# Optimization experiments

Hardware: AMD Instinct MI355X
Metric: run time of the kernel (lower is better)

## Reference

```python
import jax, jax.numpy as jnp
import numpy as np

NEG_SLOPE = 0.2
N_NODES = 50000


def _gat_layer(x, src, dst, invalid, W, al, ar, b):
    # x: [N, Fin]; src/dst: [E] (self-loops appended); invalid: [E] bool
    N = x.shape[0]
    H, F = al.shape
    z = (x @ W).reshape(N, H, F)                       # [N,H,F]
    el = jnp.sum(z * al[None], axis=-1)                # [N,H]
    er = jnp.sum(z * ar[None], axis=-1)                # [N,H]
    e = el[src] + er[dst]                              # [E,H]
    e = jnp.where(e > 0, e, NEG_SLOPE * e)             # LeakyReLU(0.2)
    e = jnp.where(invalid[:, None], -jnp.inf, e)       # removed self-loop edges
    # edge softmax per destination node (every node has a self-loop -> max finite)
    m = jax.ops.segment_max(e, dst, num_segments=N)    # [N,H]
    ex = jnp.exp(e - m[dst])
    ex = jnp.where(invalid[:, None], 0.0, ex)
    s = jax.ops.segment_sum(ex, dst, num_segments=N)   # [N,H]
    alpha = ex / s[dst]                                # [E,H]
    msg = z[src] * alpha[:, :, None]                   # [E,H,F]
    out = jax.ops.segment_sum(msg, dst, num_segments=N)  # [N,H,F]
    out = out + b.reshape(1, H, F)
    return jax.nn.elu(out)


def _with_self_loops(src, dst):
    N = N_NODES
    loop = jnp.arange(N, dtype=src.dtype)
    invalid = jnp.concatenate([src == dst, jnp.zeros(N, dtype=bool)])
    return jnp.concatenate([src, loop]), jnp.concatenate([dst, loop]), invalid


def setup_inputs() -> dict:
    key = jax.random.key(0)
    ks = jax.random.split(key, 12)
    N, Fin, H0, F0, H1, C = N_NODES, 256, 4, 32, 1, 40
    E = 800000
    sc = lambda k, shp, fan: jax.random.normal(k, shp, jnp.float32) * (1.0 / np.sqrt(fan))
    return {
        "x": jax.random.normal(ks[0], (N, Fin), jnp.float32),
        "src": jax.random.randint(ks[1], (E,), 0, N, jnp.int32),
        "dst": jax.random.randint(ks[2], (E,), 0, N, jnp.int32),
        "W0": sc(ks[3], (Fin, H0 * F0), Fin),
        "al0": sc(ks[4], (H0, F0), F0),
        "ar0": sc(ks[5], (H0, F0), F0),
        "b0": jnp.zeros((H0 * F0,), jnp.float32),
        "W1": sc(ks[6], (H0 * F0, H1 * C), H0 * F0),
        "al1": sc(ks[7], (H1, C), C),
        "ar1": sc(ks[8], (H1, C), C),
        "b1": jnp.zeros((C,), jnp.float32),
    }


def reference(x, src, dst, W0, al0, ar0, b0, W1, al1, ar1, b1):
    s, d, invalid = _with_self_loops(src, dst)
    h = _gat_layer(x, s, d, invalid, W0, al0, ar0, b0)   # [N,4,32]
    h = h.reshape(h.shape[0], -1)                        # flatten(1) -> [N,128]
    h = _gat_layer(h, s, d, invalid, W1, al1, ar1, b1)   # [N,1,40]
    return h.mean(axis=1)                                # mean over heads -> [N,40]
```

## Files before the change

### kernel.cpp

```cpp
#include <hip/hip_runtime.h>
#include <stdint.h>

#define NN 50000
#define EE 800000
#define CAP 96
#define NXCD 8
#define NPX 6250
#define EPB 2048
#define NCHUNK 391

typedef __bf16 bf16x8 __attribute__((ext_vector_type(8)));
typedef float  f32x4  __attribute__((ext_vector_type(4)));

__device__ __forceinline__ float bflo(unsigned int w){ union{unsigned int i;float f;}c; c.i=w<<16; return c.f; }
__device__ __forceinline__ float bfhi(unsigned int w){ union{unsigned int i;float f;}c; c.i=w&0xFFFF0000u; return c.f; }
__device__ __forceinline__ bf16x8 bf8_zero(){
  bf16x8 v;
  #pragma unroll
  for (int j=0;j<8;++j) v[j]=(__bf16)0.f;
  return v;
}

__global__ void k_init(int* __restrict__ cursor, int* __restrict__ csrv){
  int i = blockIdx.x*256 + threadIdx.x;
  if (i < NN){
    cursor[i] = 1;
    csrv[(size_t)i*CAP] = i;
  }
}

__global__ __launch_bounds__(256) void k_scatter(const int* __restrict__ src,
    const int* __restrict__ dst, int* __restrict__ cursor, int* __restrict__ csrv){
  const int xcd = blockIdx.x & 7;
  const int chunk = blockIdx.x >> 3;
  const int lo = xcd*NPX, hi = lo + NPX;
  int e = chunk*EPB + threadIdx.x;
  #pragma unroll
  for (int it=0; it<EPB/256; ++it, e += 256){
    if (e < EE){
      int d = dst[e];
      if (d >= lo && d < hi){
        int s = src[e];
        unsigned int inv = (s==d) ? 0x80000000u : 0u;
        int pos = atomicAdd(&cursor[d], 1);
        csrv[(size_t)d*CAP + pos] = (int)((unsigned int)s | inv);
      }
    }
  }
}

__global__ __launch_bounds__(256) void k_prepW0(const float* __restrict__ W0,
                                                __bf16* __restrict__ Wg){
  int tg = blockIdx.x*256 + threadIdx.x;
  if (tg >= 4096) return;
  int k8 = tg >> 7, n = tg & 127;
  bf16x8 v;
  #pragma unroll
  for (int j=0;j<8;++j) v[j] = (__bf16)W0[(k8*8+j)*128 + n];
  *(bf16x8*)(Wg + ((size_t)(k8*128 + n))*8) = v;
}

__global__ __launch_bounds__(256) void k_gemm0(const float* __restrict__ x,
    const __bf16* __restrict__ Wg, const float* __restrict__ al0, const float* __restrict__ ar0,
    __bf16* __restrict__ z0b, float* __restrict__ el0, float* __restrict__ er0){
  const int tid = threadIdx.x;
  const int wv = tid >> 6, ln = tid & 63, q = ln >> 4, mr = ln & 15;
  const int nhalf = wv & 1, mhalf = wv >> 1;
  const int m0w = blockIdx.x*64 + mhalf*32;
  const int n0w = nhalf*64;
  f32x4 acc[2][4];
  #pragma unroll
  for (int mt=0;mt<2;++mt)
    #pragma unroll
    for (int nt=0;nt<4;++nt) acc[mt][nt] = (f32x4){0.f,0.f,0.f,0.f};
  const bool av0 = (m0w + mr) < NN;
  const bool av1 = (m0w + 16 + mr) < NN;
  const float* xr0 = x + (size_t)(m0w + mr)*256;
  const float* xr1 = x + (size_t)(m0w + 16 + mr)*256;
  #pragma unroll
  for (int kc=0;kc<8;++kc){
    int ko = kc*32 + q*8;
    bf16x8 a0 = bf8_zero(), a1 = bf8_zero();
    if (av0){
      float4 p = *(const float4*)(xr0 + ko);
      float4 p2 = *(const float4*)(xr0 + ko + 4);
      a0[0]=(__bf16)p.x; a0[1]=(__bf16)p.y; a0[2]=(__bf16)p.z; a0[3]=(__bf16)p.w;
      a0[4]=(__bf16)p2.x; a0[5]=(__bf16)p2.y; a0[6]=(__bf16)p2.z; a0[7]=(__bf16)p2.w;
    }
    if (av1){
      float4 p = *(const float4*)(xr1 + ko);
      float4 p2 = *(const float4*)(xr1 + ko + 4);
      a1[0]=(__bf16)p.x; a1[1]=(__bf16)p.y; a1[2]=(__bf16)p.z; a1[3]=(__bf16)p.w;
      a1[4]=(__bf16)p2.x; a1[5]=(__bf16)p2.y; a1[6]=(__bf16)p2.z; a1[7]=(__bf16)p2.w;
    }
    const __bf16* wb = Wg + ((size_t)((kc*4+q)*128 + n0w + mr))*8;
    #pragma unroll
    for (int nt=0;nt<4;++nt){
      bf16x8 bf = *(const bf16x8*)(wb + (size_t)nt*16*8);
      acc[0][nt] = __builtin_amdgcn_mfma_f32_16x16x32_bf16(a0, bf, acc[0][nt], 0,0,0);
      acc[1][nt] = __builtin_amdgcn_mfma_f32_16x16x32_bf16(a1, bf, acc[1][nt], 0,0,0);
    }
  }
  float alv[4], arv[4];
  #pragma unroll
  for (int nt=0;nt<4;++nt){ int c = n0w + nt*16 + mr; alv[nt]=al0[c]; arv[nt]=ar0[c]; }
  #pragma unroll
  for (int mt=0;mt<2;++mt){
    #pragma unroll
    for (int r=0;r<4;++r){
      int grow = m0w + mt*16 + q*4 + r;
      if (grow < NN){
        #pragma unroll
        for (int nt=0;nt<4;++nt)
          z0b[(size_t)grow*128 + n0w + nt*16 + mr] = (__bf16)acc[mt][nt][r];
      }
      float pl0 = acc[mt][0][r]*alv[0] + acc[mt][1][r]*alv[1];
      float pr0 = acc[mt][0][r]*arv[0] + acc[mt][1][r]*arv[1];
      float pl1 = acc[mt][2][r]*alv[2] + acc[mt][3][r]*alv[3];
      float pr1 = acc[mt][2][r]*arv[2] + acc[mt][3][r]*arv[3];
      #pragma unroll
      for (int off=1; off<16; off<<=1){
        pl0 += __shfl_xor(pl0, off, 16); pr0 += __shfl_xor(pr0, off, 16);
        pl1 += __shfl_xor(pl1, off, 16); pr1 += __shfl_xor(pr1, off, 16);
      }
      if (mr==0 && grow<NN){
        el0[grow*4 + 2*nhalf]   = pl0; er0[grow*4 + 2*nhalf]   = pr0;
        el0[grow*4 + 2*nhalf+1] = pl1; er0[grow*4 + 2*nhalf+1] = pr1;
      }
    }
  }
}

__global__ __launch_bounds__(256) void k_agg0(const unsigned short* __restrict__ z0b,
    const float* __restrict__ el0, const float* __restrict__ er0,
    const int* __restrict__ cursor, const int* __restrict__ csrv,
    const float* __restrict__ b0, unsigned short* __restrict__ hb){
  int lane = threadIdx.x & 63;
  int i = blockIdx.x*4 + (threadIdx.x >> 6);
  int h1 = lane >> 4;
  float erv = er0[i*4 + h1];
  float ax=0.f, ay=0.f, s=0.f;
  int p = i*CAP, pe = p + cursor[i];
  for (; p+4<=pe; p+=4){
    int v0=csrv[p], v1=csrv[p+1], v2=csrv[p+2], v3=csrv[p+3];
    int u0=v0&0x7FFFFFFF, u1=v1&0x7FFFFFFF, u2=v2&0x7FFFFFFF, u3=v3&0x7FFFFFFF;
    float l0=el0[u0*4+h1], l1=el0[u1*4+h1], l2=el0[u2*4+h1], l3=el0[u3*4+h1];
    unsigned int zw0 = *(const unsigned int*)(z0b + (size_t)u0*128 + (lane<<1));
    unsigned int zw1 = *(const unsigned int*)(z0b + (size_t)u1*128 + (lane<<1));
    unsigned int zw2 = *(const unsigned int*)(z0b + (size_t)u2*128 + (lane<<1));
    unsigned int zw3 = *(const unsigned int*)(z0b + (size_t)u3*128 + (lane<<1));
    float e0=l0+erv; e0 = e0>0.f?e0:0.2f*e0; float w0 = v0>=0 ? __expf(e0) : 0.f;
    float e1=l1+erv; e1 = e1>0.f?e1:0.2f*e1; float w1 = v1>=0 ? __expf(e1) : 0.f;
    float e2=l2+erv; e2 = e2>0.f?e2:0.2f*e2; float w2 = v2>=0 ? __expf(e2) : 0.f;
    float e3=l3+erv; e3 = e3>0.f?e3:0.2f*e3; float w3 = v3>=0 ? __expf(e3) : 0.f;
    s += (w0+w1)+(w2+w3);
    ax = fmaf(w0, bflo(zw0), ax); ay = fmaf(w0, bfhi(zw0), ay);
    ax = fmaf(w1, bflo(zw1), ax); ay = fmaf(w1, bfhi(zw1), ay);
    ax = fmaf(w2, bflo(zw2), ax); ay = fmaf(w2, bfhi(zw2), ay);
    ax = fmaf(w3, bflo(zw3), ax); ay = fmaf(w3, bfhi(zw3), ay);
  }
  for (; p<pe; ++p){
    int v=csrv[p]; int u=v&0x7FFFFFFF;
    float l=el0[u*4+h1];
    unsigned int zw = *(const unsigned int*)(z0b + (size_t)u*128 + (lane<<1));
    float e=l+erv; e = e>0.f?e:0.2f*e; float w = v>=0 ? __expf(e) : 0.f;
    s += w; ax = fmaf(w, bflo(zw), ax); ay = fmaf(w, bfhi(zw), ay);
  }
  float inv = 1.f/s;
  float ox = ax*inv + b0[lane*2], oy = ay*inv + b0[lane*2+1];
  ox = ox>0.f?ox:__expf(ox)-1.f; oy = oy>0.f?oy:__expf(oy)-1.f;
  union { __bf16 b[2]; unsigned int u; } pk;
  pk.b[0]=(__bf16)ox; pk.b[1]=(__bf16)oy;
  *(unsigned int*)(hb + (size_t)i*128 + (lane<<1)) = pk.u;
}

__global__ __launch_bounds__(256) void k_gemm1(const __bf16* __restrict__ hb,
    const float* __restrict__ W1, const float* __restrict__ al1, const float* __restrict__ ar1,
    __bf16* __restrict__ z1b, float* __restrict__ el1, float* __restrict__ er1){
  __shared__ __bf16 Blds[16][48][8];
  const int tid = threadIdx.x;
  for (int t=tid; t<16*48*8; t+=256) (&Blds[0][0][0])[t] = (__bf16)0.f;
  __syncthreads();
  for (int t=tid; t<5120; t+=256){
    int k = t/40, n = t - k*40;
    Blds[k>>3][n][k&7] = (__bf16)W1[t];
  }
  __syncthreads();
  const int wm = tid >> 6, ln = tid & 63, q = ln >> 4, mr = ln & 15;
  const int m0 = blockIdx.x*64 + wm*16;
  const int arow = m0 + mr;
  const bool av = (arow < NN);
  f32x4 acc[3];
  #pragma unroll
  for (int nt=0;nt<3;++nt) acc[nt] = (f32x4){0.f,0.f,0.f,0.f};
  #pragma unroll
  for (int kc=0;kc<4;++kc){
    bf16x8 af = bf8_zero();
    if (av) af = *(const bf16x8*)(hb + (size_t)arow*128 + kc*32 + q*8);
    #pragma unroll
    for (int nt=0;nt<3;++nt){
      bf16x8 bf = *(const bf16x8*)&Blds[kc*4+q][nt*16+mr][0];
      acc[nt] = __builtin_amdgcn_mfma_f32_16x16x32_bf16(af, bf, acc[nt], 0,0,0);
    }
  }
  float alv[3], arv[3];
  #pragma unroll
  for (int nt=0;nt<3;++nt){
    int c = nt*16+mr;
    alv[nt] = (c<40) ? al1[c] : 0.f;
    arv[nt] = (c<40) ? ar1[c] : 0.f;
  }
  #pragma unroll
  for (int r=0;r<4;++r){
    int grow = m0 + q*4 + r;
    if (grow < NN){
      #pragma unroll
      for (int nt=0;nt<3;++nt){
        int c = nt*16+mr;
        if (c < 40) z1b[(size_t)grow*40 + c] = (__bf16)acc[nt][r];
      }
    }
    float pl = acc[0][r]*alv[0] + acc[1][r]*alv[1] + acc[2][r]*alv[2];
    float pr = acc[0][r]*arv[0] + acc[1][r]*arv[1] + acc[2][r]*arv[2];
    #pragma unroll
    for (int off=1; off<16; off<<=1){ pl += __shfl_xor(pl, off, 16); pr += __shfl_xor(pr, off, 16); }
    if (mr==0 && grow<NN){ el1[grow]=pl; er1[grow]=pr; }
  }
}

__global__ __launch_bounds__(256) void k_agg1(const unsigned short* __restrict__ z1b,
    const float* __restrict__ el1, const float* __restrict__ er1,
    const int* __restrict__ cursor, const int* __restrict__ csrv,
    const float* __restrict__ b1, float* __restrict__ out){
  int lane = threadIdx.x & 63;
  int i = blockIdx.x*4 + (threadIdx.x >> 6);
  int fl = (lane < 20) ? lane : 0;
  float eri = er1[i];
  float ax=0.f, ay=0.f, s=0.f;
  int p = i*CAP, pe = p + cursor[i];
  for (; p+4<=pe; p+=4){
    int v0=csrv[p], v1=csrv[p+1], v2=csrv[p+2], v3=csrv[p+3];
    int u0=v0&0x7FFFFFFF, u1=v1&0x7FFFFFFF, u2=v2&0x7FFFFFFF, u3=v3&0x7FFFFFFF;
    float l0=el1[u0], l1=el1[u1], l2=el1[u2], l3=el1[u3];
    unsigned int zw0 = *(const unsigned int*)(z1b + (size_t)u0*40 + (fl<<1));
    unsigned int zw1 = *(const unsigned int*)(z1b + (size_t)u1*40 + (fl<<1));
    unsigned int zw2 = *(const unsigned int*)(z1b + (size_t)u2*40 + (fl<<1));
    unsigned int zw3 = *(const unsigned int*)(z1b + (size_t)u3*40 + (fl<<1));
    float e0=l0+eri; e0=e0>0.f?e0:0.2f*e0; float w0 = v0>=0 ? __expf(e0) : 0.f;
    float e1=l1+eri; e1=e1>0.f?e1:0.2f*e1; float w1 = v1>=0 ? __expf(e1) : 0.f;
    float e2=l2+eri; e2=e2>0.f?e2:0.2f*e2; float w2 = v2>=0 ? __expf(e2) : 0.f;
    float e3=l3+eri; e3=e3>0.f?e3:0.2f*e3; float w3 = v3>=0 ? __expf(e3) : 0.f;
    s += (w0+w1)+(w2+w3);
    ax = fmaf(w0, bflo(zw0), ax); ay = fmaf(w0, bfhi(zw0), ay);
    ax = fmaf(w1, bflo(zw1), ax); ay = fmaf(w1, bfhi(zw1), ay);
    ax = fmaf(w2, bflo(zw2), ax); ay = fmaf(w2, bfhi(zw2), ay);
    ax = fmaf(w3, bflo(zw3), ax); ay = fmaf(w3, bfhi(zw3), ay);
  }
  for (; p<pe; ++p){
    int v=csrv[p]; int u=v&0x7FFFFFFF;
    float l=el1[u];
    unsigned int zw = *(const unsigned int*)(z1b + (size_t)u*40 + (fl<<1));
    float e=l+eri; e=e>0.f?e:0.2f*e; float w = v>=0 ? __expf(e) : 0.f;
    s += w; ax = fmaf(w, bflo(zw), ax); ay = fmaf(w, bfhi(zw), ay);
  }
  if (lane < 20){
    float inv = 1.f/s;
    float ox = ax*inv + b1[lane*2], oy = ay*inv + b1[lane*2+1];
    ox = ox>0.f?ox:__expf(ox)-1.f; oy = oy>0.f?oy:__expf(oy)-1.f;
    *(float2*)(out + (size_t)i*40 + (lane<<1)) = make_float2(ox, oy);
  }
}

extern "C" void kernel_launch(void* const* d_in, const int* in_sizes, int n_in,
                              void* d_out, int out_size, void* d_ws, size_t ws_size,
                              hipStream_t stream){
  const float* x   = (const float*)d_in[0];
  const int*   src = (const int*)d_in[1];
  const int*   dst = (const int*)d_in[2];
  const float* W0  = (const float*)d_in[3];
  const float* al0 = (const float*)d_in[4];
  const float* ar0 = (const float*)d_in[5];
  const float* b0  = (const float*)d_in[6];
  const float* W1  = (const float*)d_in[7];
  const float* al1 = (const float*)d_in[8];
  const float* ar1 = (const float*)d_in[9];
  const float* b1  = (const float*)d_in[10];
  float* out = (float*)d_out;

  __bf16* z0b = (__bf16*)d_ws;
  __bf16* hb  = z0b + (size_t)NN*128;
  __bf16* z1b = hb  + (size_t)NN*128;
  __bf16* Wg  = z1b + (size_t)NN*40;
  float* el0 = (float*)(Wg + 32768);
  float* er0 = el0 + (size_t)NN*4;
  float* el1 = er0 + (size_t)NN*4;
  float* er1 = el1 + NN;
  int* cursor = (int*)(er1 + NN);
  int* csrv   = cursor + NN;

  k_prepW0 <<<16, 256, 0, stream>>>(W0, Wg);
  k_init   <<<(NN+255)/256, 256, 0, stream>>>(cursor, csrv);
  k_scatter<<<NCHUNK*NXCD, 256, 0, stream>>>(src, dst, cursor, csrv);

  k_gemm0<<<(NN+63)/64, 256, 0, stream>>>(x, Wg, al0, ar0, z0b, el0, er0);
  k_agg0 <<<NN/4, 256, 0, stream>>>((const unsigned short*)z0b, el0, er0, cursor, csrv, b0, (unsigned short*)hb);
  k_gemm1<<<(NN+63)/64, 256, 0, stream>>>(hb, W1, al1, ar1, z1b, el1, er1);
  k_agg1 <<<NN/4, 256, 0, stream>>>((const unsigned short*)z1b, el1, er1, cursor, csrv, b1, out);
}
```

Measured before the change: 263.4 us.

## Precompute layer-0 edge attention weights during scatter and shrink per-node capacity

The CSR bucket init moves into the first GEMM, and the edge scatter now runs after that GEMM. The scatter then computes the four per-head exp(LeakyReLU) edge weights and stores them as bf16 next to each CSR slot, so the layer-0 aggregation no longer gathers el0 by source or evaluates exp per lane. Aggregation loops unroll by 8, and the per-node capacity drops from 96 to 48 to shrink the CSR footprint. The risks are bf16 rounding of the unnormalised weights, buffer overflow if any node's in-degree plus its self-loop exceeds 48, and a serial dependency that stops the scatter from overlapping the GEMM.

```diff
diff --git a/kernel.cpp b/kernel.cpp
--- a/kernel.cpp
+++ b/kernel.cpp
@@ -3,7 +3,7 @@
 
 #define NN 50000
 #define EE 800000
-#define CAP 96
+#define CAP 48
 #define NXCD 8
 #define NPX 6250
 #define EPB 2048
@@ -14,39 +14,12 @@
 
 __device__ __forceinline__ float bflo(unsigned int w){ union{unsigned int i;float f;}c; c.i=w<<16; return c.f; }
 __device__ __forceinline__ float bfhi(unsigned int w){ union{unsigned int i;float f;}c; c.i=w&0xFFFF0000u; return c.f; }
+__device__ __forceinline__ float bfs(unsigned short u){ union{unsigned int i;float f;}c; c.i=((unsigned int)u)<<16; return c.f; }
 __device__ __forceinline__ bf16x8 bf8_zero(){
   bf16x8 v;
   #pragma unroll
   for (int j=0;j<8;++j) v[j]=(__bf16)0.f;
   return v;
-}
-
-__global__ void k_init(int* __restrict__ cursor, int* __restrict__ csrv){
-  int i = blockIdx.x*256 + threadIdx.x;
-  if (i < NN){
-    cursor[i] = 1;
-    csrv[(size_t)i*CAP] = i;
-  }
-}
-
-__global__ __launch_bounds__(256) void k_scatter(const int* __restrict__ src,
-    const int* __restrict__ dst, int* __restrict__ cursor, int* __restrict__ csrv){
-  const int xcd = blockIdx.x & 7;
-  const int chunk = blockIdx.x >> 3;
-  const int lo = xcd*NPX, hi = lo + NPX;
-  int e = chunk*EPB + threadIdx.x;
-  #pragma unroll
-  for (int it=0; it<EPB/256; ++it, e += 256){
-    if (e < EE){
-      int d = dst[e];
-      if (d >= lo && d < hi){
-        int s = src[e];
-        unsigned int inv = (s==d) ? 0x80000000u : 0u;
-        int pos = atomicAdd(&cursor[d], 1);
-        csrv[(size_t)d*CAP + pos] = (int)((unsigned int)s | inv);
-      }
-    }
-  }
 }
 
 __global__ __launch_bounds__(256) void k_prepW0(const float* __restrict__ W0,
@@ -62,7 +35,8 @@
 
 __global__ __launch_bounds__(256) void k_gemm0(const float* __restrict__ x,
     const __bf16* __restrict__ Wg, const float* __restrict__ al0, const float* __restrict__ ar0,
-    __bf16* __restrict__ z0b, float* __restrict__ el0, float* __restrict__ er0){
+    __bf16* __restrict__ z0b, float* __restrict__ el0, float* __restrict__ er0,
+    unsigned short* __restrict__ wt, int* __restrict__ cursor, int* __restrict__ csrv){
   const int tid = threadIdx.x;
   const int wv = tid >> 6, ln = tid & 63, q = ln >> 4, mr = ln & 15;
   const int nhalf = wv & 1, mhalf = wv >> 1;
@@ -117,7 +91,7 @@
       float pl0 = acc[mt][0][r]*alv[0] + acc[mt][1][r]*alv[1];
       float pr0 = acc[mt][0][r]*arv[0] + acc[mt][1][r]*arv[1];
       float pl1 = acc[mt][2][r]*alv[2] + acc[mt][3][r]*alv[3];
-      float pr1 = acc[mt][2][r]*arv[2] + acc[mt][3][r]*arv[3];
+      float pr1 = acc[mt][3][r]*arv[3] + acc[mt][2][r]*arv[2];
       #pragma unroll
       for (int off=1; off<16; off<<=1){
         pl0 += __shfl_xor(pl0, off, 16); pr0 += __shfl_xor(pr0, off, 16);
@@ -126,44 +100,82 @@
       if (mr==0 && grow<NN){
         el0[grow*4 + 2*nhalf]   = pl0; er0[grow*4 + 2*nhalf]   = pr0;
         el0[grow*4 + 2*nhalf+1] = pl1; er0[grow*4 + 2*nhalf+1] = pr1;
+        float e0 = pl0 + pr0; e0 = e0>0.f ? e0 : 0.2f*e0;
+        float e1 = pl1 + pr1; e1 = e1>0.f ? e1 : 0.2f*e1;
+        union { __bf16 b[2]; unsigned int u; } pk;
+        pk.b[0]=(__bf16)__expf(e0); pk.b[1]=(__bf16)__expf(e1);
+        *(unsigned int*)(wt + ((size_t)grow*CAP)*4 + 2*nhalf) = pk.u;
+        if (nhalf==0){ csrv[(size_t)grow*CAP] = grow; cursor[grow] = 1; }
+      }
+    }
+  }
+}
+
+__global__ __launch_bounds__(256) void k_scatter(const int* __restrict__ src,
+    const int* __restrict__ dst, const float* __restrict__ el0, const float* __restrict__ er0,
+    int* __restrict__ cursor, int* __restrict__ csrv, unsigned short* __restrict__ wt){
+  const int xcd = blockIdx.x & 7;
+  const int chunk = blockIdx.x >> 3;
+  const int lo = xcd*NPX, hi = lo + NPX;
+  int e = chunk*EPB + threadIdx.x;
+  #pragma unroll
+  for (int it=0; it<EPB/256; ++it, e += 256){
+    if (e < EE){
+      int d = dst[e];
+      if (d >= lo && d < hi){
+        int s = src[e];
+        bool inv = (s==d);
+        float4 ls = *(const float4*)(el0 + (size_t)s*4);
+        float4 rd = *(const float4*)(er0 + (size_t)d*4);
+        float e0=ls.x+rd.x; e0 = e0>0.f?e0:0.2f*e0;
+        float e1=ls.y+rd.y; e1 = e1>0.f?e1:0.2f*e1;
+        float e2=ls.z+rd.z; e2 = e2>0.f?e2:0.2f*e2;
+        float e3=ls.w+rd.w; e3 = e3>0.f?e3:0.2f*e3;
+        float w0 = inv?0.f:__expf(e0), w1 = inv?0.f:__expf(e1);
+        float w2 = inv?0.f:__expf(e2), w3 = inv?0.f:__expf(e3);
+        int pos = atomicAdd(&cursor[d], 1);
+        size_t slot = (size_t)d*CAP + pos;
+        csrv[slot] = (int)((unsigned int)s | (inv?0x80000000u:0u));
+        union { __bf16 b[4]; uint2 u; } pk;
+        pk.b[0]=(__bf16)w0; pk.b[1]=(__bf16)w1; pk.b[2]=(__bf16)w2; pk.b[3]=(__bf16)w3;
+        *(uint2*)(wt + slot*4) = pk.u;
       }
     }
   }
 }
 
 __global__ __launch_bounds__(256) void k_agg0(const unsigned short* __restrict__ z0b,
-    const float* __restrict__ el0, const float* __restrict__ er0,
+    const unsigned short* __restrict__ wt,
     const int* __restrict__ cursor, const int* __restrict__ csrv,
     const float* __restrict__ b0, unsigned short* __restrict__ hb){
   int lane = threadIdx.x & 63;
   int i = blockIdx.x*4 + (threadIdx.x >> 6);
   int h1 = lane >> 4;
-  float erv = er0[i*4 + h1];
+  int lane2 = lane << 1;
   float ax=0.f, ay=0.f, s=0.f;
   int p = i*CAP, pe = p + cursor[i];
+  for (; p+8<=pe; p+=8){
+    #pragma unroll
+    for (int j=0;j<8;++j){
+      int u = csrv[p+j] & 0x7FFFFFFF;
+      float w = bfs(wt[(size_t)(p+j)*4 + h1]);
+      unsigned int zw = *(const unsigned int*)(z0b + (size_t)u*128 + lane2);
+      s += w; ax = fmaf(w, bflo(zw), ax); ay = fmaf(w, bfhi(zw), ay);
+    }
+  }
   for (; p+4<=pe; p+=4){
-    int v0=csrv[p], v1=csrv[p+1], v2=csrv[p+2], v3=csrv[p+3];
-    int u0=v0&0x7FFFFFFF, u1=v1&0x7FFFFFFF, u2=v2&0x7FFFFFFF, u3=v3&0x7FFFFFFF;
-    float l0=el0[u0*4+h1], l1=el0[u1*4+h1], l2=el0[u2*4+h1], l3=el0[u3*4+h1];
-    unsigned int zw0 = *(const unsigned int*)(z0b + (size_t)u0*128 + (lane<<1));
-    unsigned int zw1 = *(const unsigned int*)(z0b + (size_t)u1*128 + (lane<<1));
-    unsigned int zw2 = *(const unsigned int*)(z0b + (size_t)u2*128 + (lane<<1));
-    unsigned int zw3 = *(const unsigned int*)(z0b + (size_t)u3*128 + (lane<<1));
-    float e0=l0+erv; e0 = e0>0.f?e0:0.2f*e0; float w0 = v0>=0 ? __expf(e0) : 0.f;
-    float e1=l1+erv; e1 = e1>0.f?e1:0.2f*e1; float w1 = v1>=0 ? __expf(e1) : 0.f;
-    float e2=l2+erv; e2 = e2>0.f?e2:0.2f*e2; float w2 = v2>=0 ? __expf(e2) : 0.f;
-    float e3=l3+erv; e3 = e3>0.f?e3:0.2f*e3; float w3 = v3>=0 ? __expf(e3) : 0.f;
-    s += (w0+w1)+(w2+w3);
-    ax = fmaf(w0, bflo(zw0), ax); ay = fmaf(w0, bfhi(zw0), ay);
-    ax = fmaf(w1, bflo(zw1), ax); ay = fmaf(w1, bfhi(zw1), ay);
-    ax = fmaf(w2, bflo(zw2), ax); ay = fmaf(w2, bfhi(zw2), ay);
-    ax = fmaf(w3, bflo(zw3), ax); ay = fmaf(w3, bfhi(zw3), ay);
+    #pragma unroll
+    for (int j=0;j<4;++j){
+      int u = csrv[p+j] & 0x7FFFFFFF;
+      float w = bfs(wt[(size_t)(p+j)*4 + h1]);
+      unsigned int zw = *(const unsigned int*)(z0b + (size_t)u*128 + lane2);
+      s += w; ax = fmaf(w, bflo(zw), ax); ay = fmaf(w, bfhi(zw), ay);
+    }
   }
   for (; p<pe; ++p){
-    int v=csrv[p]; int u=v&0x7FFFFFFF;
-    float l=el0[u*4+h1];
-    unsigned int zw = *(const unsigned int*)(z0b + (size_t)u*128 + (lane<<1));
-    float e=l+erv; e = e>0.f?e:0.2f*e; float w = v>=0 ? __expf(e) : 0.f;
+    int u = csrv[p] & 0x7FFFFFFF;
+    float w = bfs(wt[(size_t)p*4 + h1]);
+    unsigned int zw = *(const unsigned int*)(z0b + (size_t)u*128 + lane2);
     s += w; ax = fmaf(w, bflo(zw), ax); ay = fmaf(w, bfhi(zw), ay);
   }
   float inv = 1.f/s;
@@ -171,7 +183,7 @@
   ox = ox>0.f?ox:__expf(ox)-1.f; oy = oy>0.f?oy:__expf(oy)-1.f;
   union { __bf16 b[2]; unsigned int u; } pk;
   pk.b[0]=(__bf16)ox; pk.b[1]=(__bf16)oy;
-  *(unsigned int*)(hb + (size_t)i*128 + (lane<<1)) = pk.u;
+  *(unsigned int*)(hb + (size_t)i*128 + lane2) = pk.u;
 }
 
 __global__ __launch_bounds__(256) void k_gemm1(const __bf16* __restrict__ hb,
@@ -234,32 +246,34 @@
     const float* __restrict__ b1, float* __restrict__ out){
   int lane = threadIdx.x & 63;
   int i = blockIdx.x*4 + (threadIdx.x >> 6);
-  int fl = (lane < 20) ? lane : 0;
+  int fl = (lane < 20) ? (lane<<1) : 0;
   float eri = er1[i];
   float ax=0.f, ay=0.f, s=0.f;
   int p = i*CAP, pe = p + cursor[i];
+  for (; p+8<=pe; p+=8){
+    #pragma unroll
+    for (int j=0;j<8;++j){
+      int v=csrv[p+j]; int u=v&0x7FFFFFFF;
+      float l=el1[u];
+      unsigned int zw = *(const unsigned int*)(z1b + (size_t)u*40 + fl);
+      float e=l+eri; e=e>0.f?e:0.2f*e; float w = v>=0 ? __expf(e) : 0.f;
+      s += w; ax = fmaf(w, bflo(zw), ax); ay = fmaf(w, bfhi(zw), ay);
+    }
+  }
   for (; p+4<=pe; p+=4){
-    int v0=csrv[p], v1=csrv[p+1], v2=csrv[p+2], v3=csrv[p+3];
-    int u0=v0&0x7FFFFFFF, u1=v1&0x7FFFFFFF, u2=v2&0x7FFFFFFF, u3=v3&0x7FFFFFFF;
-    float l0=el1[u0], l1=el1[u1], l2=el1[u2], l3=el1[u3];
-    unsigned int zw0 = *(const unsigned int*)(z1b + (size_t)u0*40 + (fl<<1));
-    unsigned int zw1 = *(const unsigned int*)(z1b + (size_t)u1*40 + (fl<<1));
-    unsigned int zw2 = *(const unsigned int*)(z1b + (size_t)u2*40 + (fl<<1));
-    unsigned int zw3 = *(const unsigned int*)(z1b + (size_t)u3*40 + (fl<<1));
-    float e0=l0+eri; e0=e0>0.f?e0:0.2f*e0; float w0 = v0>=0 ? __expf(e0) : 0.f;
-    float e1=l1+eri; e1=e1>0.f?e1:0.2f*e1; float w1 = v1>=0 ? __expf(e1) : 0.f;
-    float e2=l2+eri; e2=e2>0.f?e2:0.2f*e2; float w2 = v2>=0 ? __expf(e2) : 0.f;
-    float e3=l3+eri; e3=e3>0.f?e3:0.2f*e3; float w3 = v3>=0 ? __expf(e3) : 0.f;
-    s += (w0+w1)+(w2+w3);
-    ax = fmaf(w0, bflo(zw0), ax); ay = fmaf(w0, bfhi(zw0), ay);
-    ax = fmaf(w1, bflo(zw1), ax); ay = fmaf(w1, bfhi(zw1), ay);
-    ax = fmaf(w2, bflo(zw2), ax); ay = fmaf(w2, bfhi(zw2), ay);
-    ax = fmaf(w3, bflo(zw3), ax); ay = fmaf(w3, bfhi(zw3), ay);
+    #pragma unroll
+    for (int j=0;j<4;++j){
+      int v=csrv[p+j]; int u=v&0x7FFFFFFF;
+      float l=el1[u];
+      unsigned int zw = *(const unsigned int*)(z1b + (size_t)u*40 + fl);
+      float e=l+eri; e=e>0.f?e:0.2f*e; float w = v>=0 ? __expf(e) : 0.f;
+      s += w; ax = fmaf(w, bflo(zw), ax); ay = fmaf(w, bfhi(zw), ay);
+    }
   }
   for (; p<pe; ++p){
     int v=csrv[p]; int u=v&0x7FFFFFFF;
     float l=el1[u];
-    unsigned int zw = *(const unsigned int*)(z1b + (size_t)u*40 + (fl<<1));
+    unsigned int zw = *(const unsigned int*)(z1b + (size_t)u*40 + fl);
     float e=l+eri; e=e>0.f?e:0.2f*e; float w = v>=0 ? __expf(e) : 0.f;
     s += w; ax = fmaf(w, bflo(zw), ax); ay = fmaf(w, bfhi(zw), ay);
   }
@@ -291,7 +305,8 @@
   __bf16* hb  = z0b + (size_t)NN*128;
   __bf16* z1b = hb  + (size_t)NN*128;
   __bf16* Wg  = z1b + (size_t)NN*40;
-  float* el0 = (float*)(Wg + 32768);
+  unsigned short* wt = (unsigned short*)(Wg + 32768);
+  float* el0 = (float*)(wt + (size_t)NN*CAP*4);
   float* er0 = el0 + (size_t)NN*4;
   float* el1 = er0 + (size_t)NN*4;
   float* er1 = el1 + NN;
@@ -299,11 +314,9 @@
   int* csrv   = cursor + NN;
 
   k_prepW0 <<<16, 256, 0, stream>>>(W0, Wg);
-  k_init   <<<(NN+255)/256, 256, 0, stream>>>(cursor, csrv);
-  k_scatter<<<NCHUNK*NXCD, 256, 0, stream>>>(src, dst, cursor, csrv);
-
-  k_gemm0<<<(NN+63)/64, 256, 0, stream>>>(x, Wg, al0, ar0, z0b, el0, er0);
-  k_agg0 <<<NN/4, 256, 0, stream>>>((const unsigned short*)z0b, el0, er0, cursor, csrv, b0, (unsigned short*)hb);
+  k_gemm0<<<(NN+63)/64, 256, 0, stream>>>(x, Wg, al0, ar0, z0b, el0, er0, wt, cursor, csrv);
+  k_scatter<<<NCHUNK*NXCD, 256, 0, stream>>>(src, dst, el0, er0, cursor, csrv, wt);
+  k_agg0 <<<NN/4, 256, 0, stream>>>((const unsigned short*)z0b, wt, cursor, csrv, b0, (unsigned short*)hb);
   k_gemm1<<<(NN+63)/64, 256, 0, stream>>>(hb, W1, al1, ar1, z1b, el1, er1);
   k_agg1 <<<NN/4, 256, 0, stream>>>((const unsigned short*)z1b, el1, er1, cursor, csrv, b1, out);
 }
```

Result: slower. 301.9 us (+14.6%).
